# Kernel optimization log

Measured on AMD Instinct MI355X. Metric: run time of the kernel, lower is better.

The kernel has to match this reference:

```python
import jax, jax.numpy as jnp
import numpy as np

N = 30000   # nodes
E = 240000  # edges
G = 16      # graphs in batch
DIMS = [1, 256, 512, 1024]
OUT = 1024

def _xavier(key, fan_in, fan_out):
    lim = float(np.sqrt(6.0 / (fan_in + fan_out)))
    return jax.random.uniform(key, (fan_in, fan_out), minval=-lim, maxval=lim, dtype=jnp.float32)

def setup_inputs() -> dict:
    key = jax.random.key(0)
    ks = jax.random.split(key, 8)
    x = jax.random.normal(ks[0], (N, DIMS[0]), dtype=jnp.float32)
    edge_index = jax.random.randint(ks[1], (2, E), 0, N, dtype=jnp.int64)
    batch = jnp.sort(jax.random.randint(ks[2], (N,), 0, G, dtype=jnp.int64))
    W1 = _xavier(ks[3], DIMS[0], DIMS[1]); b1 = jnp.zeros((DIMS[1],), jnp.float32)
    W2 = _xavier(ks[4], DIMS[1], DIMS[2]); b2 = jnp.zeros((DIMS[2],), jnp.float32)
    W3 = _xavier(ks[5], DIMS[2], DIMS[3]); b3 = jnp.zeros((DIMS[3],), jnp.float32)
    Wo = _xavier(ks[6], DIMS[3], OUT);     bo = jnp.zeros((OUT,), jnp.float32)
    return {"x": x, "edge_index": edge_index, "batch": batch,
            "W1": W1, "b1": b1, "W2": W2, "b2": b2, "W3": W3, "b3": b3,
            "Wo": Wo, "bo": bo}

def reference(x, edge_index, batch, W1, b1, W2, b2, W3, b3, Wo, bo):
    n = x.shape[0]
    loops = jnp.arange(n)
    # GCNConv adds self-loops, then symmetric deg^-1/2 normalization
    src = jnp.concatenate([edge_index[0], loops])
    dst = jnp.concatenate([edge_index[1], loops])
    deg = jnp.zeros((n,), jnp.float32).at[dst].add(1.0)  # >=1 due to self-loops
    dis = jax.lax.rsqrt(deg)
    norm = (dis[src] * dis[dst])[:, None]  # [E+N, 1]

    def gcn(h, W, b):
        h = h @ W                                   # linear (no bias in lin)
        agg = jnp.zeros_like(h).at[dst].add(h[src] * norm)  # scatter-add messages
        return agg + b                              # GCNConv bias

    h = jax.nn.relu(gcn(x, W1, b1))
    h = jax.nn.relu(gcn(h, W2, b2))
    h = jax.nn.relu(gcn(h, W3, b3))
    # global mean pool over graphs
    sums = jnp.zeros((G, h.shape[1]), h.dtype).at[batch].add(h)
    cnt = jnp.zeros((G,), h.dtype).at[batch].add(1.0)
    pooled = sums / jnp.maximum(cnt, 1.0)[:, None]
    return pooled @ Wo + bo
```

## Files before the change

### kernel.cpp

```cpp
#include <hip/hip_runtime.h>
#include <hip/hip_bf16.h>
#include <stdint.h>

#define N_NODES 30000
#define E_EDGES 240000
#define NGRAPH  16
#define D1      256
#define D2      512
#define D3      1024
#define DOUT    1024
#define M_PAD   30720
#define NT_M    240
#define CAP     40

typedef unsigned short ushort_t;
typedef short short8 __attribute__((ext_vector_type(8)));
typedef float f32x4 __attribute__((ext_vector_type(4)));

__device__ __forceinline__ float bf2f(ushort_t u) {
    union { unsigned int i; float f; } v; v.i = ((unsigned int)u) << 16; return v.f;
}
__device__ __forceinline__ ushort_t f2bf(float x) {
    union { float f; unsigned int i; } v; v.f = x;
    unsigned int r = v.i + 0x7fffu + ((v.i >> 16) & 1u);
    return (ushort_t)(r >> 16);
}

__global__ void k_detect(const void* w1, const void* ei, int* flags) {
    int lane = threadIdx.x & 63;
    const ushort_t* h = (const ushort_t*)w1;
    float v = fabsf(bf2f(h[lane * 2]));
    unsigned long long badf = __ballot(!(v <= 0.25f));
    const int* e = (const int*)ei;
    unsigned long long badi = __ballot(e[lane * 2 + 1] != 0);
    if (threadIdx.x == 0) {
        flags[0] = (badf == 0ull) ? 1 : 0;
        flags[1] = (badi == 0ull) ? 1 : 0;
    }
}

__global__ void k_setup(const void* x, const void* batch, const void* w1, const void* b1,
                        const void* b2, const void* b3, const void* bo,
                        const void* W2, const void* W3,
                        float* xf, int* batch32, float* W1f, float* b1f, float* b2f,
                        float* b3f, float* bof, ushort_t* Wt2, ushort_t* Wt3,
                        int* slotcnt, float* pooled, float* pooled2, const int* flags) {
    int isbf = flags[0];
    int bid = blockIdx.x;
    int tid = threadIdx.x;
    if (bid < 492) {
        int i = bid * 256 + tid;
        if (i < 3072) {
            const void* src; float* dst; int idx;
            if      (i < 256)  { src = w1; dst = W1f; idx = i; }
            else if (i < 512)  { src = b1; dst = b1f; idx = i - 256; }
            else if (i < 1024) { src = b2; dst = b2f; idx = i - 512; }
            else if (i < 2048) { src = b3; dst = b3f; idx = i - 1024; }
            else               { src = bo; dst = bof; idx = i - 2048; }
            dst[idx] = isbf ? bf2f(((const ushort_t*)src)[idx]) : ((const float*)src)[idx];
        } else if (i < 33072) {
            int idx = i - 3072;
            xf[idx] = isbf ? bf2f(((const ushort_t*)x)[idx]) : ((const float*)x)[idx];
        } else if (i < 63072) {
            int idx = i - 33072;
            batch32[idx] = flags[1] ? (int)((const long long*)batch)[idx]
                                    : ((const int*)batch)[idx];
        } else if (i < 93072) {
            slotcnt[i - 63072] = 0;
        } else if (i < 109456) {
            pooled[i - 93072] = 0.0f;
        } else if (i < 125840) {
            pooled2[i - 109456] = 0.0f;
        }
    } else {
        __shared__ ushort_t tile[32][33];
        int tb = bid - 492;
        const void* in; ushort_t* out; int R, C, bx, by;
        if (tb < 128) { in = W2; out = Wt2; R = D1; C = D2; bx = tb & 15; by = tb >> 4; }
        else { tb -= 128; in = W3; out = Wt3; R = D2; C = D3; bx = tb & 31; by = tb >> 5; }
        int tx = tid & 31, ty = tid >> 5;
        int c0 = bx * 32, r0 = by * 32;
        for (int i = ty; i < 32; i += 8) {
            size_t idx = (size_t)(r0 + i) * C + c0 + tx;
            tile[i][tx] = isbf ? ((const ushort_t*)in)[idx] : f2bf(((const float*)in)[idx]);
        }
        __syncthreads();
        for (int i = ty; i < 32; i += 8) out[(size_t)(c0 + i) * R + r0 + tx] = tile[tx][i];
    }
}

__global__ void k_edge_count(const void* ei, int* slotcnt, int* slots, const int* flags) {
    int e = blockIdx.x * 256 + threadIdx.x;
    if (e >= E_EDGES) return;
    int s, d;
    if (flags[1]) {
        s = (int)((const long long*)ei)[e];
        d = (int)((const long long*)ei)[E_EDGES + e];
    } else {
        s = ((const int*)ei)[e];
        d = ((const int*)ei)[E_EDGES + e];
    }
    if ((unsigned)s >= N_NODES || (unsigned)d >= N_NODES) return;
    int pos = atomicAdd(&slotcnt[d], 1);
    if (pos < CAP) slots[d * CAP + pos] = s;
}

__global__ void k_s1(const float* xf, const int* slotcnt, const int* slots,
                     const int* batch, float* dis, float* s1, float* cntg) {
    int b = blockIdx.x;
    if (b == 118) {
        int g = threadIdx.x;
        if (g >= NGRAPH) return;
        int lo0 = 0, hi0 = N_NODES;
        while (lo0 < hi0) { int m = (lo0 + hi0) >> 1; if (batch[m] < g) lo0 = m + 1; else hi0 = m; }
        int lo1 = lo0, hi1 = N_NODES;
        while (lo1 < hi1) { int m = (lo1 + hi1) >> 1; if (batch[m] < g + 1) lo1 = m + 1; else hi1 = m; }
        cntg[g] = (float)(lo1 - lo0);
        return;
    }
    int d = b * 256 + threadIdx.x;
    if (d >= N_NODES) return;
    int cd = slotcnt[d];
    float di = rsqrtf(1.0f + (float)cd);
    dis[d] = di;
    int cnt = cd < CAP ? cd : CAP;
    float acc = xf[d] * di;
    for (int k = 0; k < cnt; k++) {
        int s = slots[d * CAP + k];
        acc += xf[s] * rsqrtf(1.0f + (float)slotcnt[s]);
    }
    s1[d] = acc * di;
}

__global__ void k_agg1(const float* s1, const float* W1f, const float* b1f,
                       ushort_t* a2, const int* slots, const int* slotcnt, const float* dis) {
    int node = blockIdx.x * 4 + (threadIdx.x >> 6);
    int lane = threadIdx.x & 63;
    int c4 = lane * 4;
    float w[4], bb[4], a[4];
    #pragma unroll
    for (int j = 0; j < 4; j++) { w[j] = W1f[c4 + j]; bb[j] = b1f[c4 + j]; }
    float di = dis[node];
    int cnt = slotcnt[node]; cnt = cnt < CAP ? cnt : CAP;
    int s_l = (lane < cnt) ? slots[node * CAP + lane] : 0;
    float wn_l = dis[s_l] * di;
    float ss_l = s1[s_l];
    float sv = s1[node];
    float wsl = di * di;
    #pragma unroll
    for (int j = 0; j < 4; j++) a[j] = wsl * fmaxf(sv * w[j] + bb[j], 0.0f);
    for (int k = 0; k < cnt; k++) {
        float ss = __shfl(ss_l, k);
        float wn = __shfl(wn_l, k);
        #pragma unroll
        for (int j = 0; j < 4; j++) a[j] += wn * fmaxf(ss * w[j] + bb[j], 0.0f);
    }
    uint2 o;
    o.x = (unsigned int)f2bf(a[0]) | ((unsigned int)f2bf(a[1]) << 16);
    o.y = (unsigned int)f2bf(a[2]) | ((unsigned int)f2bf(a[3]) << 16);
    *(uint2*)&a2[(size_t)node * D1 + c4] = o;
}

__global__ void k_agg2(const ushort_t* h, ushort_t* out, const int* slots,
                       const int* slotcnt, const float* dis) {
    int node = blockIdx.x * 4 + (threadIdx.x >> 6);
    int lane = threadIdx.x & 63;
    int c8 = lane * 8;
    float di = dis[node];
    int cnt = slotcnt[node]; cnt = cnt < CAP ? cnt : CAP;
    int s_l = (lane < cnt) ? slots[node * CAP + lane] : 0;
    float ws_l = dis[s_l] * di;
    float w = di * di;
    const ushort_t* hp = h + c8;
    short8 p = *(const short8*)&hp[(size_t)node * D2];
    float a[8];
    #pragma unroll
    for (int j = 0; j < 8; j++) a[j] = w * bf2f((ushort_t)p[j]);
    if (cnt > 0) {
        int s0 = __shfl(s_l, 0);
        float ws0 = __shfl(ws_l, 0);
        short8 q0 = *(const short8*)&hp[(size_t)s0 * D2];
        for (int k = 1; k < cnt; k++) {
            int sk = __shfl(s_l, k);
            float ws1 = __shfl(ws_l, k);
            short8 q1 = *(const short8*)&hp[(size_t)sk * D2];
            #pragma unroll
            for (int j = 0; j < 8; j++) a[j] += ws0 * bf2f((ushort_t)q0[j]);
            q0 = q1; ws0 = ws1;
        }
        #pragma unroll
        for (int j = 0; j < 8; j++) a[j] += ws0 * bf2f((ushort_t)q0[j]);
    }
    uint4 o;
    o.x = (unsigned int)f2bf(a[0]) | ((unsigned int)f2bf(a[1]) << 16);
    o.y = (unsigned int)f2bf(a[2]) | ((unsigned int)f2bf(a[3]) << 16);
    o.z = (unsigned int)f2bf(a[4]) | ((unsigned int)f2bf(a[5]) << 16);
    o.w = (unsigned int)f2bf(a[6]) | ((unsigned int)f2bf(a[7]) << 16);
    *(uint4*)&out[(size_t)node * D2 + c8] = o;
}

__global__ __launch_bounds__(256, 4) void k_gemm(const ushort_t* A, const ushort_t* Bt,
                                                 const float* bias, ushort_t* Cmat,
                                                 int K, int Ncols, int ntn) {
    __shared__ __align__(16) ushort_t As[2][128 * 32];
    __shared__ __align__(16) ushort_t Bs[2][128 * 32];
    int tid = threadIdx.x;
    int id = blockIdx.x;
    int xcd = id & 7, q = id >> 3;
    int rt = xcd * (NT_M / 8) + q / ntn;
    int ct = q % ntn;
    int bm0 = rt * 128, bn0 = ct * 128;
    int wave = tid >> 6, lane = tid & 63;
    int wm = (wave & 1) * 64, wn = (wave >> 1) * 64;
    int l15 = lane & 15, quad = lane >> 4;

    int m1 = tid >> 2, kc = tid & 3, k1 = kc << 3;
    int m2 = m1 + 64;
    int wsw = (kc ^ ((m1 >> 1) & 3)) << 3;
    int off1 = m1 * 32 + wsw, off2 = off1 + 64 * 32;
    const ushort_t* pA1 = A + (size_t)(bm0 + m1) * K + k1;
    const ushort_t* pA2 = A + (size_t)(bm0 + m2) * K + k1;
    const ushort_t* pB1 = Bt + (size_t)(bn0 + m1) * K + k1;
    const ushort_t* pB2 = Bt + (size_t)(bn0 + m2) * K + k1;

    {
        uint4 la0 = *(const uint4*)pA1, la1 = *(const uint4*)pA2;
        uint4 lb0 = *(const uint4*)pB1, lb1 = *(const uint4*)pB2;
        *(uint4*)&As[0][off1] = la0; *(uint4*)&As[0][off2] = la1;
        *(uint4*)&Bs[0][off1] = lb0; *(uint4*)&Bs[0][off2] = lb1;
    }

    int rsw = (quad ^ ((l15 >> 1) & 3)) << 3;

    f32x4 acc[4][4];
    for (int a = 0; a < 4; a++)
        for (int b = 0; b < 4; b++)
            acc[a][b] = (f32x4){0.f, 0.f, 0.f, 0.f};

    int niter = K >> 5;
    for (int it = 0; it < niter; ++it) {
        __syncthreads();
        int ktn = (it + 1) << 5;
        uint4 na0, na1, nb0, nb1;
        if (ktn < K) {
            na0 = *(const uint4*)(pA1 + ktn); na1 = *(const uint4*)(pA2 + ktn);
            nb0 = *(const uint4*)(pB1 + ktn); nb1 = *(const uint4*)(pB2 + ktn);
        }
        int cb = it & 1;
        short8 af[4], bfr[4];
        for (int im = 0; im < 4; im++)
            af[im] = *(const short8*)&As[cb][(wm + im * 16 + l15) * 32 + rsw];
        for (int in = 0; in < 4; in++)
            bfr[in] = *(const short8*)&Bs[cb][(wn + in * 16 + l15) * 32 + rsw];
        for (int im = 0; im < 4; im++)
            for (int in = 0; in < 4; in++)
                acc[im][in] = __builtin_amdgcn_mfma_f32_16x16x32_bf16(af[im], bfr[in], acc[im][in], 0, 0, 0);
        if (ktn < K) {
            int wb = cb ^ 1;
            *(uint4*)&As[wb][off1] = na0; *(uint4*)&As[wb][off2] = na1;
            *(uint4*)&Bs[wb][off1] = nb0; *(uint4*)&Bs[wb][off2] = nb1;
        }
    }

    for (int im = 0; im < 4; im++) {
        int row = bm0 + wm + im * 16 + quad * 4;
        for (int in = 0; in < 4; in++) {
            int col = bn0 + wn + in * 16 + l15;
            float bv = bias[col];
            for (int r = 0; r < 4; r++) {
                float v = acc[im][in][r] + bv;
                v = v > 0.0f ? v : 0.0f;
                Cmat[(size_t)(row + r) * Ncols + col] = f2bf(v);
            }
        }
    }
}

__global__ __launch_bounds__(256, 4) void k_gemm_pool(const ushort_t* A, const ushort_t* Bt,
                                                      const float* bias, const int* batch,
                                                      float* pooled, int K, int ntn) {
    __shared__ __align__(16) ushort_t As[2][128 * 32];
    __shared__ __align__(16) ushort_t Bs[2][128 * 32];
    int tid = threadIdx.x;
    int id = blockIdx.x;
    int xcd = id & 7, q = id >> 3;
    int rt = xcd * (NT_M / 8) + q / ntn;
    int ct = q % ntn;
    int bm0 = rt * 128, bn0 = ct * 128;
    int wave = tid >> 6, lane = tid & 63;
    int wm = (wave & 1) * 64, wn = (wave >> 1) * 64;
    int l15 = lane & 15, quad = lane >> 4;

    int m1 = tid >> 2, kc = tid & 3, k1 = kc << 3;
    int m2 = m1 + 64;
    int wsw = (kc ^ ((m1 >> 1) & 3)) << 3;
    int off1 = m1 * 32 + wsw, off2 = off1 + 64 * 32;
    const ushort_t* pA1 = A + (size_t)(bm0 + m1) * K + k1;
    const ushort_t* pA2 = A + (size_t)(bm0 + m2) * K + k1;
    const ushort_t* pB1 = Bt + (size_t)(bn0 + m1) * K + k1;
    const ushort_t* pB2 = Bt + (size_t)(bn0 + m2) * K + k1;

    {
        uint4 la0 = *(const uint4*)pA1, la1 = *(const uint4*)pA2;
        uint4 lb0 = *(const uint4*)pB1, lb1 = *(const uint4*)pB2;
        *(uint4*)&As[0][off1] = la0; *(uint4*)&As[0][off2] = la1;
        *(uint4*)&Bs[0][off1] = lb0; *(uint4*)&Bs[0][off2] = lb1;
    }

    int rsw = (quad ^ ((l15 >> 1) & 3)) << 3;

    f32x4 acc[4][4];
    for (int a = 0; a < 4; a++)
        for (int b = 0; b < 4; b++)
            acc[a][b] = (f32x4){0.f, 0.f, 0.f, 0.f};

    int niter = K >> 5;
    for (int it = 0; it < niter; ++it) {
        __syncthreads();
        int ktn = (it + 1) << 5;
        uint4 na0, na1, nb0, nb1;
        if (ktn < K) {
            na0 = *(const uint4*)(pA1 + ktn); na1 = *(const uint4*)(pA2 + ktn);
            nb0 = *(const uint4*)(pB1 + ktn); nb1 = *(const uint4*)(pB2 + ktn);
        }
        int cb = it & 1;
        short8 af[4], bfr[4];
        for (int im = 0; im < 4; im++)
            af[im] = *(const short8*)&As[cb][(wm + im * 16 + l15) * 32 + rsw];
        for (int in = 0; in < 4; in++)
            bfr[in] = *(const short8*)&Bs[cb][(wn + in * 16 + l15) * 32 + rsw];
        for (int im = 0; im < 4; im++)
            for (int in = 0; in < 4; in++)
                acc[im][in] = __builtin_amdgcn_mfma_f32_16x16x32_bf16(af[im], bfr[in], acc[im][in], 0, 0, 0);
        if (ktn < K) {
            int wb = cb ^ 1;
            *(uint4*)&As[wb][off1] = na0; *(uint4*)&As[wb][off2] = na1;
            *(uint4*)&Bs[wb][off1] = nb0; *(uint4*)&Bs[wb][off2] = nb1;
        }
    }

    __syncthreads();
    float* pl = (float*)&As[0][0];
    int* gtile = (int*)&Bs[0][0];
    for (int i = tid; i < NGRAPH * 128; i += 256) pl[i] = 0.0f;
    if (tid < 128) {
        int r = bm0 + tid; if (r > N_NODES - 1) r = N_NODES - 1;
        int g = batch[r]; g = g < 0 ? 0 : (g > NGRAPH - 1 ? NGRAPH - 1 : g);
        gtile[tid] = g;
    }
    __syncthreads();

    int gmin = gtile[0], gmax = gtile[127];
    if (gmin == gmax && bm0 + 127 < N_NODES) {
        float csum[4];
        #pragma unroll
        for (int in = 0; in < 4; in++) csum[in] = 0.0f;
        for (int im = 0; im < 4; im++) {
            #pragma unroll
            for (int in = 0; in < 4; in++) {
                float bv = bias[bn0 + wn + in * 16 + l15];
                #pragma unroll
                for (int r = 0; r < 4; r++)
                    csum[in] += fmaxf(acc[im][in][r] + bv, 0.0f);
            }
        }
        #pragma unroll
        for (int in = 0; in < 4; in++) {
            csum[in] += __shfl_xor(csum[in], 16);
            csum[in] += __shfl_xor(csum[in], 32);
        }
        if (quad == 0) {
            #pragma unroll
            for (int in = 0; in < 4; in++)
                atomicAdd(&pl[gmin * 128 + wn + in * 16 + l15], csum[in]);
        }
    } else {
        for (int im = 0; im < 4; im++) {
            int rl = wm + im * 16 + quad * 4;
            for (int in = 0; in < 4; in++) {
                int cl = wn + in * 16 + l15;
                float bv = bias[bn0 + cl];
                float vsum = 0.0f;
                int gprev = gtile[rl];
                for (int r = 0; r < 4; r++) {
                    int row = bm0 + rl + r;
                    float v = (row < N_NODES) ? fmaxf(acc[im][in][r] + bv, 0.0f) : 0.0f;
                    int g = gtile[rl + r];
                    if (g != gprev) {
                        atomicAdd(&pl[gprev * 128 + cl], vsum);
                        vsum = 0.0f; gprev = g;
                    }
                    vsum += v;
                }
                atomicAdd(&pl[gprev * 128 + cl], vsum);
            }
        }
    }
    __syncthreads();

    int span = (gmax - gmin + 1) * 128;
    for (int idx = tid; idx < span; idx += 256) {
        int g = gmin + (idx >> 7), cl = idx & 127;
        float v = pl[g * 128 + cl];
        if (v != 0.0f) atomicAdd(&pooled[g * DOUT + bn0 + cl], v);
    }
}

__global__ __launch_bounds__(256) void k_out_partial(const float* pooled, const void* Wo,
                                                     float* pooled2, const int* flags) {
    __shared__ float pl[NGRAPH * 32];
    int tid = threadIdx.x;
    int col = blockIdx.x * 256 + tid;
    int k0 = blockIdx.y * 32;
    for (int i = tid; i < NGRAPH * 32; i += 256) {
        int g = i >> 5, kk = i & 31;
        pl[i] = pooled[g * D3 + k0 + kk];
    }
    __syncthreads();
    int isbf = flags[0];
    float acc[NGRAPH];
    #pragma unroll
    for (int g = 0; g < NGRAPH; g++) acc[g] = 0.0f;
    #pragma unroll 4
    for (int kk = 0; kk < 32; kk++) {
        int k = k0 + kk;
        float wv = isbf ? bf2f(((const ushort_t*)Wo)[(size_t)k * DOUT + col])
                        : ((const float*)Wo)[(size_t)k * DOUT + col];
        #pragma unroll
        for (int g = 0; g < NGRAPH; g++)
            acc[g] += pl[g * 32 + kk] * wv;
    }
    #pragma unroll
    for (int g = 0; g < NGRAPH; g++)
        atomicAdd(&pooled2[g * DOUT + col], acc[g]);
}

__global__ void k_out_fin(const float* pooled2, const float* bof, const float* cntg,
                          void* out, const int* flags) {
    int i = blockIdx.x * 256 + threadIdx.x;
    int g = i >> 10, o = i & 1023;
    float c = cntg[g]; c = c > 1.0f ? c : 1.0f;
    float v = pooled2[i] / c + bof[o];
    if (flags[0]) ((ushort_t*)out)[i] = f2bf(v);
    else          ((float*)out)[i] = v;
}

extern "C" void kernel_launch(void* const* d_in, const int* in_sizes, int n_in,
                              void* d_out, int out_size, void* d_ws, size_t ws_size,
                              hipStream_t stream) {
    const void* x_raw  = d_in[0];
    const void* ei_raw = d_in[1];
    const void* b_raw  = d_in[2];
    const void* W1_raw = d_in[3];
    const void* b1_raw = d_in[4];
    const void* W2_raw = d_in[5];
    const void* b2_raw = d_in[6];
    const void* W3_raw = d_in[7];
    const void* b3_raw = d_in[8];
    const void* Wo_raw = d_in[9];
    const void* bo_raw = d_in[10];

    char* w = (char*)d_ws;
    size_t off = 0;
    auto alloc = [&](size_t b) { size_t o = off; off += (b + 255) & ~(size_t)255; return o; };
    int*   flags   = (int*)  (w + alloc(256));
    float* xf      = (float*)(w + alloc((size_t)N_NODES * 4));
    int*   batch32 = (int*)  (w + alloc((size_t)N_NODES * 4));
    float* W1f     = (float*)(w + alloc(D1 * 4));
    float* b1f     = (float*)(w + alloc(D1 * 4));
    float* b2f     = (float*)(w + alloc(D2 * 4));
    float* b3f     = (float*)(w + alloc(D3 * 4));
    float* bof     = (float*)(w + alloc(DOUT * 4));
    float* dis     = (float*)(w + alloc((size_t)N_NODES * 4));
    float* s1      = (float*)(w + alloc((size_t)N_NODES * 4));
    float* cntg    = (float*)(w + alloc(64));
    float* pooled  = (float*)(w + alloc((size_t)NGRAPH * DOUT * 4));
    float* pooled2 = (float*)(w + alloc((size_t)NGRAPH * DOUT * 4));
    int*   slotcnt = (int*)  (w + alloc((size_t)N_NODES * 4));
    int*   slots   = (int*)  (w + alloc((size_t)N_NODES * CAP * 4));
    ushort_t* Wt2  = (ushort_t*)(w + alloc((size_t)D2 * D1 * 2));
    ushort_t* Wt3  = (ushort_t*)(w + alloc((size_t)D3 * D2 * 2));
    ushort_t* slabA = (ushort_t*)(w + alloc((size_t)M_PAD * D2 * 2));
    ushort_t* a2 = slabA;
    ushort_t* a3 = slabA;
    ushort_t* h2   = (ushort_t*)(w + alloc((size_t)M_PAD * D2 * 2));

    int nb_e = (E_EDGES + 255) / 256;

    k_detect<<<1, 64, 0, stream>>>(W1_raw, ei_raw, flags);
    k_setup<<<1132, 256, 0, stream>>>(x_raw, b_raw, W1_raw, b1_raw, b2_raw, b3_raw, bo_raw,
                                      W2_raw, W3_raw, xf, batch32, W1f, b1f, b2f, b3f, bof,
                                      Wt2, Wt3, slotcnt, pooled, pooled2, flags);
    k_edge_count<<<nb_e, 256, 0, stream>>>(ei_raw, slotcnt, slots, flags);
    k_s1<<<119, 256, 0, stream>>>(xf, slotcnt, slots, batch32, dis, s1, cntg);

    k_agg1<<<N_NODES / 4, 256, 0, stream>>>(s1, W1f, b1f, a2, slots, slotcnt, dis);
    k_gemm<<<NT_M * (D2 / 128), 256, 0, stream>>>(a2, Wt2, b2f, h2, D1, D2, D2 / 128);
    k_agg2<<<N_NODES / 4, 256, 0, stream>>>(h2, a3, slots, slotcnt, dis);
    k_gemm_pool<<<NT_M * (D3 / 128), 256, 0, stream>>>(a3, Wt3, b3f, batch32, pooled, D2, D3 / 128);

    k_out_partial<<<dim3(DOUT / 256, D3 / 32), 256, 0, stream>>>(pooled, Wo_raw, pooled2, flags);
    k_out_fin<<<NGRAPH * DOUT / 256, 256, 0, stream>>>(pooled2, bof, cntg, d_out, flags);
}
```

Measured before the change: 234.4 us.

## Inline dtype detection per wave and restructure GEMM double-buffer loop

Removes the separate k_detect launch: each wave now runs the ballot-based bf16/int64 detection itself, so the flags buffer and one kernel launch go away. The two GEMM kernels are rewritten into a manually unrolled-by-two double-buffered loop. It keeps two register prefetch sets, issues global loads one stage further ahead, and uses raw s_barrier with lgkmcnt waits instead of __syncthreads. Launch bounds drop from 4 to 3 waves per SIMD to make room for the extra registers, which may lower occupancy. The unroll by two assumes K/32 is even, which holds for K of 256 and 512.

```diff
diff --git a/kernel.cpp b/kernel.cpp
--- a/kernel.cpp
+++ b/kernel.cpp
@@ -26,26 +26,23 @@
     return (ushort_t)(r >> 16);
 }
 
-__global__ void k_detect(const void* w1, const void* ei, int* flags) {
+__device__ __forceinline__ int wave_isbf(const void* w1) {
     int lane = threadIdx.x & 63;
-    const ushort_t* h = (const ushort_t*)w1;
-    float v = fabsf(bf2f(h[lane * 2]));
-    unsigned long long badf = __ballot(!(v <= 0.25f));
-    const int* e = (const int*)ei;
-    unsigned long long badi = __ballot(e[lane * 2 + 1] != 0);
-    if (threadIdx.x == 0) {
-        flags[0] = (badf == 0ull) ? 1 : 0;
-        flags[1] = (badi == 0ull) ? 1 : 0;
-    }
+    float v = fabsf(bf2f(((const ushort_t*)w1)[lane * 2]));
+    return __ballot(!(v <= 0.25f)) == 0ull;
+}
+__device__ __forceinline__ int wave_isi64(const void* ei) {
+    int lane = threadIdx.x & 63;
+    return __ballot(((const int*)ei)[lane * 2 + 1] != 0) == 0ull;
 }
 
 __global__ void k_setup(const void* x, const void* batch, const void* w1, const void* b1,
                         const void* b2, const void* b3, const void* bo,
-                        const void* W2, const void* W3,
+                        const void* W2, const void* W3, const void* ei,
                         float* xf, int* batch32, float* W1f, float* b1f, float* b2f,
                         float* b3f, float* bof, ushort_t* Wt2, ushort_t* Wt3,
-                        int* slotcnt, float* pooled, float* pooled2, const int* flags) {
-    int isbf = flags[0];
+                        int* slotcnt, float* pooled, float* pooled2) {
+    int isbf = wave_isbf(w1);
     int bid = blockIdx.x;
     int tid = threadIdx.x;
     if (bid < 492) {
@@ -63,8 +60,9 @@
             xf[idx] = isbf ? bf2f(((const ushort_t*)x)[idx]) : ((const float*)x)[idx];
         } else if (i < 63072) {
             int idx = i - 33072;
-            batch32[idx] = flags[1] ? (int)((const long long*)batch)[idx]
-                                    : ((const int*)batch)[idx];
+            int isi64 = wave_isi64(ei);
+            batch32[idx] = isi64 ? (int)((const long long*)batch)[idx]
+                                 : ((const int*)batch)[idx];
         } else if (i < 93072) {
             slotcnt[i - 63072] = 0;
         } else if (i < 109456) {
@@ -89,11 +87,12 @@
     }
 }
 
-__global__ void k_edge_count(const void* ei, int* slotcnt, int* slots, const int* flags) {
+__global__ void k_edge_count(const void* ei, int* slotcnt, int* slots) {
+    int isi64 = wave_isi64(ei);
     int e = blockIdx.x * 256 + threadIdx.x;
     if (e >= E_EDGES) return;
     int s, d;
-    if (flags[1]) {
+    if (isi64) {
         s = (int)((const long long*)ei)[e];
         d = (int)((const long long*)ei)[E_EDGES + e];
     } else {
@@ -199,7 +198,68 @@
     *(uint4*)&out[(size_t)node * D2 + c8] = o;
 }
 
-__global__ __launch_bounds__(256, 4) void k_gemm(const ushort_t* A, const ushort_t* Bt,
+#define GEMM_PROLOGUE_AND_LOOP(EPILOG_SYNC)                                            \
+    uint4 ea0 = *(const uint4*)pA1, ea1 = *(const uint4*)pA2;                          \
+    uint4 eb0 = *(const uint4*)pB1, eb1 = *(const uint4*)pB2;                          \
+    *(uint4*)&As[0][off1] = ea0; *(uint4*)&As[0][off2] = ea1;                          \
+    *(uint4*)&Bs[0][off1] = eb0; *(uint4*)&Bs[0][off2] = eb1;                          \
+    uint4 oa0 = *(const uint4*)(pA1 + 32), oa1 = *(const uint4*)(pA2 + 32);            \
+    uint4 ob0 = *(const uint4*)(pB1 + 32), ob1 = *(const uint4*)(pB2 + 32);            \
+    asm volatile("s_waitcnt lgkmcnt(0)" ::: "memory");                                 \
+    __builtin_amdgcn_s_barrier();                                                      \
+    int rsw = (quad ^ ((l15 >> 1) & 3)) << 3;                                          \
+    f32x4 acc[4][4];                                                                   \
+    for (int a = 0; a < 4; a++)                                                        \
+        for (int b = 0; b < 4; b++)                                                    \
+            acc[a][b] = (f32x4){0.f, 0.f, 0.f, 0.f};                                   \
+    int niter = K >> 5;                                                                \
+    for (int t = 0; t < niter; t += 2) {                                               \
+                        \
+        int k2 = (t + 2) << 5;                                                         \
+        if (k2 < K) {                                                                  \
+            ea0 = *(const uint4*)(pA1 + k2); ea1 = *(const uint4*)(pA2 + k2);          \
+            eb0 = *(const uint4*)(pB1 + k2); eb1 = *(const uint4*)(pB2 + k2);          \
+        }                                                                              \
+        {                                                                              \
+            short8 af[4], bfr[4];                                                      \
+            for (int im = 0; im < 4; im++)                                             \
+                af[im] = *(const short8*)&As[0][(wm + im * 16 + l15) * 32 + rsw];      \
+            for (int in = 0; in < 4; in++)                                             \
+                bfr[in] = *(const short8*)&Bs[0][(wn + in * 16 + l15) * 32 + rsw];     \
+            for (int im = 0; im < 4; im++)                                             \
+                for (int in = 0; in < 4; in++)                                         \
+                    acc[im][in] = __builtin_amdgcn_mfma_f32_16x16x32_bf16(af[im], bfr[in], acc[im][in], 0, 0, 0); \
+        }                                                                              \
+        *(uint4*)&As[1][off1] = oa0; *(uint4*)&As[1][off2] = oa1;                      \
+        *(uint4*)&Bs[1][off1] = ob0; *(uint4*)&Bs[1][off2] = ob1;                      \
+        asm volatile("s_waitcnt lgkmcnt(0)" ::: "memory");                             \
+        __builtin_amdgcn_s_barrier();                                                  \
+                       \
+        int k3 = (t + 3) << 5;                                                         \
+        if (k3 < K) {                                                                  \
+            oa0 = *(const uint4*)(pA1 + k3); oa1 = *(const uint4*)(pA2 + k3);          \
+            ob0 = *(const uint4*)(pB1 + k3); ob1 = *(const uint4*)(pB2 + k3);          \
+        }                                                                              \
+        {                                                                              \
+            short8 af[4], bfr[4];                                                      \
+            for (int im = 0; im < 4; im++)                                             \
+                af[im] = *(const short8*)&As[1][(wm + im * 16 + l15) * 32 + rsw];      \
+            for (int in = 0; in < 4; in++)                                             \
+                bfr[in] = *(const short8*)&Bs[1][(wn + in * 16 + l15) * 32 + rsw];     \
+            for (int im = 0; im < 4; im++)                                             \
+                for (int in = 0; in < 4; in++)                                         \
+                    acc[im][in] = __builtin_amdgcn_mfma_f32_16x16x32_bf16(af[im], bfr[in], acc[im][in], 0, 0, 0); \
+        }                                                                              \
+        if (k2 < K) {                                                                  \
+            *(uint4*)&As[0][off1] = ea0; *(uint4*)&As[0][off2] = ea1;                  \
+            *(uint4*)&Bs[0][off1] = eb0; *(uint4*)&Bs[0][off2] = eb1;                  \
+        }                                                                              \
+        asm volatile("s_waitcnt lgkmcnt(0)" ::: "memory");                             \
+        __builtin_amdgcn_s_barrier();                                                  \
+    }                                                                                  \
+    EPILOG_SYNC
+
+__global__ __launch_bounds__(256, 3) void k_gemm(const ushort_t* A, const ushort_t* Bt,
                                                  const float* bias, ushort_t* Cmat,
                                                  int K, int Ncols, int ntn) {
     __shared__ __align__(16) ushort_t As[2][128 * 32];
@@ -215,52 +275,14 @@
     int l15 = lane & 15, quad = lane >> 4;
 
     int m1 = tid >> 2, kc = tid & 3, k1 = kc << 3;
-    int m2 = m1 + 64;
     int wsw = (kc ^ ((m1 >> 1) & 3)) << 3;
     int off1 = m1 * 32 + wsw, off2 = off1 + 64 * 32;
     const ushort_t* pA1 = A + (size_t)(bm0 + m1) * K + k1;
-    const ushort_t* pA2 = A + (size_t)(bm0 + m2) * K + k1;
+    const ushort_t* pA2 = pA1 + (size_t)64 * K;
     const ushort_t* pB1 = Bt + (size_t)(bn0 + m1) * K + k1;
-    const ushort_t* pB2 = Bt + (size_t)(bn0 + m2) * K + k1;
-
-    {
-        uint4 la0 = *(const uint4*)pA1, la1 = *(const uint4*)pA2;
-        uint4 lb0 = *(const uint4*)pB1, lb1 = *(const uint4*)pB2;
-        *(uint4*)&As[0][off1] = la0; *(uint4*)&As[0][off2] = la1;
-        *(uint4*)&Bs[0][off1] = lb0; *(uint4*)&Bs[0][off2] = lb1;
-    }
-
-    int rsw = (quad ^ ((l15 >> 1) & 3)) << 3;
-
-    f32x4 acc[4][4];
-    for (int a = 0; a < 4; a++)
-        for (int b = 0; b < 4; b++)
-            acc[a][b] = (f32x4){0.f, 0.f, 0.f, 0.f};
-
-    int niter = K >> 5;
-    for (int it = 0; it < niter; ++it) {
-        __syncthreads();
-        int ktn = (it + 1) << 5;
-        uint4 na0, na1, nb0, nb1;
-        if (ktn < K) {
-            na0 = *(const uint4*)(pA1 + ktn); na1 = *(const uint4*)(pA2 + ktn);
-            nb0 = *(const uint4*)(pB1 + ktn); nb1 = *(const uint4*)(pB2 + ktn);
-        }
-        int cb = it & 1;
-        short8 af[4], bfr[4];
-        for (int im = 0; im < 4; im++)
-            af[im] = *(const short8*)&As[cb][(wm + im * 16 + l15) * 32 + rsw];
-        for (int in = 0; in < 4; in++)
-            bfr[in] = *(const short8*)&Bs[cb][(wn + in * 16 + l15) * 32 + rsw];
-        for (int im = 0; im < 4; im++)
-            for (int in = 0; in < 4; in++)
-                acc[im][in] = __builtin_amdgcn_mfma_f32_16x16x32_bf16(af[im], bfr[in], acc[im][in], 0, 0, 0);
-        if (ktn < K) {
-            int wb = cb ^ 1;
-            *(uint4*)&As[wb][off1] = na0; *(uint4*)&As[wb][off2] = na1;
-            *(uint4*)&Bs[wb][off1] = nb0; *(uint4*)&Bs[wb][off2] = nb1;
-        }
-    }
+    const ushort_t* pB2 = pB1 + (size_t)64 * K;
+
+    GEMM_PROLOGUE_AND_LOOP()
 
     for (int im = 0; im < 4; im++) {
         int row = bm0 + wm + im * 16 + quad * 4;
@@ -276,7 +298,7 @@
     }
 }
 
-__global__ __launch_bounds__(256, 4) void k_gemm_pool(const ushort_t* A, const ushort_t* Bt,
+__global__ __launch_bounds__(256, 3) void k_gemm_pool(const ushort_t* A, const ushort_t* Bt,
                                                       const float* bias, const int* batch,
                                                       float* pooled, int K, int ntn) {
     __shared__ __align__(16) ushort_t As[2][128 * 32];
@@ -292,54 +314,15 @@
     int l15 = lane & 15, quad = lane >> 4;
 
     int m1 = tid >> 2, kc = tid & 3, k1 = kc << 3;
-    int m2 = m1 + 64;
     int wsw = (kc ^ ((m1 >> 1) & 3)) << 3;
     int off1 = m1 * 32 + wsw, off2 = off1 + 64 * 32;
     const ushort_t* pA1 = A + (size_t)(bm0 + m1) * K + k1;
-    const ushort_t* pA2 = A + (size_t)(bm0 + m2) * K + k1;
+    const ushort_t* pA2 = pA1 + (size_t)64 * K;
     const ushort_t* pB1 = Bt + (size_t)(bn0 + m1) * K + k1;
-    const ushort_t* pB2 = Bt + (size_t)(bn0 + m2) * K + k1;
-
-    {
-        uint4 la0 = *(const uint4*)pA1, la1 = *(const uint4*)pA2;
-        uint4 lb0 = *(const uint4*)pB1, lb1 = *(const uint4*)pB2;
-        *(uint4*)&As[0][off1] = la0; *(uint4*)&As[0][off2] = la1;
-        *(uint4*)&Bs[0][off1] = lb0; *(uint4*)&Bs[0][off2] = lb1;
-    }
-
-    int rsw = (quad ^ ((l15 >> 1) & 3)) << 3;
-
-    f32x4 acc[4][4];
-    for (int a = 0; a < 4; a++)
-        for (int b = 0; b < 4; b++)
-            acc[a][b] = (f32x4){0.f, 0.f, 0.f, 0.f};
-
-    int niter = K >> 5;
-    for (int it = 0; it < niter; ++it) {
-        __syncthreads();
-        int ktn = (it + 1) << 5;
-        uint4 na0, na1, nb0, nb1;
-        if (ktn < K) {
-            na0 = *(const uint4*)(pA1 + ktn); na1 = *(const uint4*)(pA2 + ktn);
-            nb0 = *(const uint4*)(pB1 + ktn); nb1 = *(const uint4*)(pB2 + ktn);
-        }
-        int cb = it & 1;
-        short8 af[4], bfr[4];
-        for (int im = 0; im < 4; im++)
-            af[im] = *(const short8*)&As[cb][(wm + im * 16 + l15) * 32 + rsw];
-        for (int in = 0; in < 4; in++)
-            bfr[in] = *(const short8*)&Bs[cb][(wn + in * 16 + l15) * 32 + rsw];
-        for (int im = 0; im < 4; im++)
-            for (int in = 0; in < 4; in++)
-                acc[im][in] = __builtin_amdgcn_mfma_f32_16x16x32_bf16(af[im], bfr[in], acc[im][in], 0, 0, 0);
-        if (ktn < K) {
-            int wb = cb ^ 1;
-            *(uint4*)&As[wb][off1] = na0; *(uint4*)&As[wb][off2] = na1;
-            *(uint4*)&Bs[wb][off1] = nb0; *(uint4*)&Bs[wb][off2] = nb1;
-        }
-    }
-
-    __syncthreads();
+    const ushort_t* pB2 = pB1 + (size_t)64 * K;
+
+    GEMM_PROLOGUE_AND_LOOP(__syncthreads();)
+
     float* pl = (float*)&As[0][0];
     int* gtile = (int*)&Bs[0][0];
     for (int i = tid; i < NGRAPH * 128; i += 256) pl[i] = 0.0f;
@@ -407,7 +390,7 @@
 }
 
 __global__ __launch_bounds__(256) void k_out_partial(const float* pooled, const void* Wo,
-                                                     float* pooled2, const int* flags) {
+                                                     float* pooled2, const void* w1) {
     __shared__ float pl[NGRAPH * 32];
     int tid = threadIdx.x;
     int col = blockIdx.x * 256 + tid;
@@ -417,7 +400,7 @@
         pl[i] = pooled[g * D3 + k0 + kk];
     }
     __syncthreads();
-    int isbf = flags[0];
+    int isbf = wave_isbf(w1);
     float acc[NGRAPH];
     #pragma unroll
     for (int g = 0; g < NGRAPH; g++) acc[g] = 0.0f;
@@ -436,13 +419,14 @@
 }
 
 __global__ void k_out_fin(const float* pooled2, const float* bof, const float* cntg,
-                          void* out, const int* flags) {
+                          void* out, const void* w1) {
+    int isbf = wave_isbf(w1);
     int i = blockIdx.x * 256 + threadIdx.x;
     int g = i >> 10, o = i & 1023;
     float c = cntg[g]; c = c > 1.0f ? c : 1.0f;
     float v = pooled2[i] / c + bof[o];
-    if (flags[0]) ((ushort_t*)out)[i] = f2bf(v);
-    else          ((float*)out)[i] = v;
+    if (isbf) ((ushort_t*)out)[i] = f2bf(v);
+    else      ((float*)out)[i] = v;
 }
 
 extern "C" void kernel_launch(void* const* d_in, const int* in_sizes, int n_in,
@@ -463,7 +447,6 @@
     char* w = (char*)d_ws;
     size_t off = 0;
     auto alloc = [&](size_t b) { size_t o = off; off += (b + 255) & ~(size_t)255; return o; };
-    int*   flags   = (int*)  (w + alloc(256));
     float* xf      = (float*)(w + alloc((size_t)N_NODES * 4));
     int*   batch32 = (int*)  (w + alloc((size_t)N_NODES * 4));
     float* W1f     = (float*)(w + alloc(D1 * 4));
@@ -487,11 +470,10 @@
 
     int nb_e = (E_EDGES + 255) / 256;
 
-    k_detect<<<1, 64, 0, stream>>>(W1_raw, ei_raw, flags);
     k_setup<<<1132, 256, 0, stream>>>(x_raw, b_raw, W1_raw, b1_raw, b2_raw, b3_raw, bo_raw,
-                                      W2_raw, W3_raw, xf, batch32, W1f, b1f, b2f, b3f, bof,
-                                      Wt2, Wt3, slotcnt, pooled, pooled2, flags);
-    k_edge_count<<<nb_e, 256, 0, stream>>>(ei_raw, slotcnt, slots, flags);
+                                      W2_raw, W3_raw, ei_raw, xf, batch32, W1f, b1f, b2f,
+                                      b3f, bof, Wt2, Wt3, slotcnt, pooled, pooled2);
+    k_edge_count<<<nb_e, 256, 0, stream>>>(ei_raw, slotcnt, slots);
     k_s1<<<119, 256, 0, stream>>>(xf, slotcnt, slots, batch32, dis, s1, cntg);
 
     k_agg1<<<N_NODES / 4, 256, 0, stream>>>(s1, W1f, b1f, a2, slots, slotcnt, dis);
@@ -499,6 +481,6 @@
     k_agg2<<<N_NODES / 4, 256, 0, stream>>>(h2, a3, slots, slotcnt, dis);
     k_gemm_pool<<<NT_M * (D3 / 128), 256, 0, stream>>>(a3, Wt3, b3f, batch32, pooled, D2, D3 / 128);
 
-    k_out_partial<<<dim3(DOUT / 256, D3 / 32), 256, 0, stream>>>(pooled, Wo_raw, pooled2, flags);
-    k_out_fin<<<NGRAPH * DOUT / 256, 256, 0, stream>>>(pooled2, bof, cntg, d_out, flags);
-}
+    k_out_partial<<<dim3(DOUT / 256, D3 / 32), 256, 0, stream>>>(pooled, Wo_raw, pooled2, W1_raw);
+    k_out_fin<<<NGRAPH * DOUT / 256, 256, 0, stream>>>(pooled2, bof, cntg, d_out, W1_raw);
+}
```

Result: no change. 232.5 us (-0.8%).
